# Optimization experiments

Hardware: AMD Instinct MI355X
Metric: run time of the kernel (lower is better)

## Reference

```python
import jax, jax.numpy as jnp
import numpy as np

N = 6144      # total residues (12 complexes x 512)
SEG = 512
NC = 14       # atom channels per residue
E = 64        # embed_size
HD = 128      # hidden_size
C = 25        # num_classes
K = 9         # k_neighbors
L = 3         # n_layers
ROUNDS = 3    # iter_round


def _forward(X, S, batch_id, embed, W_in, b_in, channel_w, eW1, eb1, eW2, eb2, cW1, cb1, cW2, cb2, nW1, nb1, nW2, nb2, mW1, mb1, mW2, mb2, oW1, ob1, oW2, ob2):
    n = X.shape[0]
    silu = jax.nn.silu
    # pairs in different complexes (or self) are never neighbors
    cross = (batch_id[:, None] != batch_id[None, :]) | jnp.eye(n, dtype=bool)
    Hmem = None
    H = None
    for t in range(ROUNDS):
        H0 = embed[S]                                    # residue embedding [N,E]
        if Hmem is not None:                             # keep_memory: memory_ffn(H_prev)
            m = silu(Hmem) @ mW1 + mb1
            H0 = H0 + (silu(m) @ mW2 + mb2)
        H = H0 @ W_in + b_in                             # [N,HD]
        # dynamic KNN edge construction on current CA coordinates (_knn_edges)
        ca = X[:, 1]                                     # [N,3]
        d2 = jnp.sum((ca[:, None, :] - ca[None, :, :]) ** 2, -1)
        d2 = jnp.where(cross, 1e9, d2)
        _, nbr = jax.lax.top_k(-d2, K)                   # [N,K] neighbor indices
        for l in range(L):                               # AMEGNN / AMEncoder layers
            Hj = H[nbr]                                  # gather [N,K,HD]
            Xj = X[nbr]                                  # gather [N,K,NC,3]
            diff = X[:, None] - Xj                       # [N,K,NC,3]
            # channel-weighted radial feature
            radial = jnp.einsum('nkcd,nkcd,c->nk', diff, diff, channel_w)[..., None]
            Hi = jnp.broadcast_to(H[:, None], Hj.shape)
            ein = jnp.concatenate([Hi, Hj, radial], -1)  # [N,K,2HD+1]
            msg = silu(silu(ein @ eW1[l] + eb1[l]) @ eW2[l] + eb2[l])
            scale = silu(msg @ cW1[l] + cb1[l]) @ cW2[l] + cb2[l]     # [N,K,1]
            X = X + jnp.mean(diff * scale[..., None], axis=1)        # equivariant coord update
            agg = jnp.sum(msg, axis=1)                   # scatter-sum over neighbors [N,HD]
            H = H + silu(jnp.concatenate([H, agg], -1) @ nW1[l] + nb1[l]) @ nW2[l] + nb2[l]
        Hmem = H
    logits = silu(silu(H) @ oW1 + ob1) @ oW2 + ob2       # ffn_residue
    return logits, X


def setup_inputs() -> dict:
    key = jax.random.key(0)
    ks = jax.random.split(key, 16)
    r = lambda i, shape, s=0.05: jax.random.normal(ks[i], shape, dtype=jnp.float32) * s
    return {
        'X': jax.random.normal(ks[0], (N, NC, 3), dtype=jnp.float32) * 3.0,
        'S': jax.random.randint(ks[1], (N,), 0, C),
        'batch_id': jnp.arange(N, dtype=jnp.int32) // SEG,
        'embed': r(2, (C, E), 1.0),
        'W_in': r(3, (E, HD)), 'b_in': jnp.zeros((HD,), jnp.float32),
        'channel_w': jax.random.uniform(ks[4], (NC,), dtype=jnp.float32),
        'eW1': r(5, (L, 2 * HD + 1, HD)), 'eb1': jnp.zeros((L, HD), jnp.float32),
        'eW2': r(6, (L, HD, HD)), 'eb2': jnp.zeros((L, HD), jnp.float32),
        'cW1': r(7, (L, HD, HD)), 'cb1': jnp.zeros((L, HD), jnp.float32),
        'cW2': r(8, (L, HD, 1)), 'cb2': jnp.zeros((L, 1), jnp.float32),
        'nW1': r(9, (L, 2 * HD, HD)), 'nb1': jnp.zeros((L, HD), jnp.float32),
        'nW2': r(10, (L, HD, HD)), 'nb2': jnp.zeros((L, HD), jnp.float32),
        'mW1': r(11, (HD, HD)), 'mb1': jnp.zeros((HD,), jnp.float32),
        'mW2': r(12, (HD, E)), 'mb2': jnp.zeros((E,), jnp.float32),
        'oW1': r(13, (HD, HD)), 'ob1': jnp.zeros((HD,), jnp.float32),
        'oW2': r(14, (HD, C)), 'ob2': jnp.zeros((C,), jnp.float32),
    }


def reference(X, S, batch_id, embed, W_in, b_in, channel_w, eW1, eb1, eW2, eb2, cW1, cb1, cW2, cb2, nW1, nb1, nW2, nb2, mW1, mb1, mW2, mb2, oW1, ob1, oW2, ob2):
    return _forward(X, S, batch_id, embed, W_in, b_in, channel_w, eW1, eb1, eW2, eb2, cW1, cb1, cW2, cb2, nW1, nb1, nW2, nb2, mW1, mb1, mW2, mb2, oW1, ob1, oW2, ob2)
```

## Files before the change

### kernel.cpp

```cpp
#include <hip/hip_runtime.h>
#include <math.h>

#define NNODE 6144
#define SEG   512
#define NCH   14
#define XD    42
#define ED    64
#define HD    128
#define NCLS  25
#define KN    9
#define NPB   7
#define ROWS  64
#define EDGE_BLOCKS ((NNODE + NPB - 1) / NPB)

typedef __attribute__((ext_vector_type(8))) short short8;
typedef __attribute__((ext_vector_type(4))) short short4v;
typedef __attribute__((ext_vector_type(4))) float f32x4;

__device__ __forceinline__ float silu_f(float x) {
  return x / (1.0f + __expf(-x));
}
__device__ __forceinline__ short f2bf(float x) {
  unsigned u = __builtin_bit_cast(unsigned, x);
  unsigned r = (u + 0x7fffu + ((u >> 16) & 1u)) >> 16;
  return (short)r;
}
__device__ __forceinline__ float bf2f(short s) {
  unsigned u = ((unsigned)(unsigned short)s) << 16;
  return __builtin_bit_cast(float, u);
}
__device__ __forceinline__ f32x4 mfma16(short8 a, short8 b, f32x4 c) {
  return __builtin_amdgcn_mfma_f32_16x16x32_bf16(a, b, c, 0, 0, 0);
}
__device__ __forceinline__ int swz128(int row, int col) {
  return row * 128 + (col ^ ((row & 7) << 3));
}
__device__ __forceinline__ int swz256(int row, int col) {
  return row * 256 + (col ^ ((row & 7) << 3));
}

__global__ __launch_bounds__(256) void prep_weights(
    const float* __restrict__ eW1, const float* __restrict__ eW2,
    const float* __restrict__ cW1, const float* __restrict__ nW1,
    const float* __restrict__ nW2, short* __restrict__ out)
{
  const int mat = blockIdx.y % 5, l = blockIdx.y / 5;
  const int idx = blockIdx.x * 256 + threadIdx.x;
  const int K = (mat == 0 || mat == 3) ? 256 : 128;
  if (idx >= K * 128) return;
  const int n = idx / K, k = idx - n * K;
  const float* src;
  switch (mat) {
    case 0: src = eW1 + (size_t)l * 257 * 128; break;
    case 1: src = eW2 + (size_t)l * 128 * 128; break;
    case 2: src = cW1 + (size_t)l * 128 * 128; break;
    case 3: src = nW1 + (size_t)l * 256 * 128; break;
    default: src = nW2 + (size_t)l * 128 * 128; break;
  }
  const int dofs[5] = {0, 32768, 49152, 65536, 98304};
  out[(size_t)l * 114688 + dofs[mat] + idx] = f2bf(src[k * 128 + n]);
}

__global__ void copy_kernel(const float* __restrict__ src, float* __restrict__ dst, int n) {
  int i = blockIdx.x * blockDim.x + threadIdx.x;
  if (i < n) dst[i] = src[i];
}

__global__ __launch_bounds__(512) void pq_kernel(
    const float* __restrict__ Hin, const short* __restrict__ W1T,
    float* __restrict__ PQ)
{
  __shared__ __align__(16) short A[16 * HD];
  const int t = threadIdx.x;
  const int m0 = blockIdx.x * 16;

  {
    const int r = t >> 5, c4 = t & 31;
    const float4 v = ((const float4*)(Hin + (size_t)m0 * HD))[r * 32 + c4];
    short4v s;
    s.x = f2bf(v.x); s.y = f2bf(v.y); s.z = f2bf(v.z); s.w = f2bf(v.w);
    *(short4v*)&A[swz128(r, c4 * 4)] = s;
  }
  __syncthreads();

  const int wid = t >> 6, lane = t & 63;
  const int lr = lane & 15, lk = lane >> 4;

  f32x4 acc[2] = {};
#pragma unroll
  for (int ks = 0; ks < 4; ++ks) {
    const int k0 = ks * 32 + lk * 8;
    const short8 a = *(const short8*)&A[swz128(lr, k0)];
#pragma unroll
    for (int ni = 0; ni < 2; ++ni) {
      const int c = (wid * 2 + ni) * 16 + lr;
      const short* bp = (c < HD) ? (W1T + c * 256 + k0)
                                 : (W1T + (c - HD) * 256 + HD + k0);
      const short8 b = *(const short8*)bp;
      acc[ni] = mfma16(a, b, acc[ni]);
    }
  }
#pragma unroll
  for (int ni = 0; ni < 2; ++ni) {
    const int c = (wid * 2 + ni) * 16 + lr;
#pragma unroll
    for (int g = 0; g < 4; ++g) {
      const int row = lk * 4 + g;
      PQ[(size_t)(m0 + row) * 256 + c] = acc[ni][g];
    }
  }
}

__global__ __launch_bounds__(128) void h_init_kernel(
    const float* __restrict__ embed, const int* __restrict__ S,
    const float* __restrict__ W_in, const float* __restrict__ b_in,
    const float* __restrict__ Hmem,
    const float* __restrict__ mW1, const float* __restrict__ mb1,
    const float* __restrict__ mW2, const float* __restrict__ mb2,
    float* __restrict__ Hout)
{
  __shared__ float a1[HD];
  __shared__ float a2[HD];
  __shared__ float h0[ED];
  const int i = blockIdx.x, j = threadIdx.x;

  if (Hmem) {
    a1[j] = silu_f(Hmem[i * HD + j]);
    __syncthreads();
    float m0 = 0.f, m1 = 0.f, m2 = 0.f, m3 = 0.f;
    for (int k = 0; k < HD; k += 4) {
      m0 = fmaf(a1[k + 0], mW1[(k + 0) * HD + j], m0);
      m1 = fmaf(a1[k + 1], mW1[(k + 1) * HD + j], m1);
      m2 = fmaf(a1[k + 2], mW1[(k + 2) * HD + j], m2);
      m3 = fmaf(a1[k + 3], mW1[(k + 3) * HD + j], m3);
    }
    a2[j] = silu_f(mb1[j] + ((m0 + m1) + (m2 + m3)));
    __syncthreads();
    if (j < ED) {
      float v0 = 0.f, v1 = 0.f, v2 = 0.f, v3 = 0.f;
      for (int k = 0; k < HD; k += 4) {
        v0 = fmaf(a2[k + 0], mW2[(k + 0) * ED + j], v0);
        v1 = fmaf(a2[k + 1], mW2[(k + 1) * ED + j], v1);
        v2 = fmaf(a2[k + 2], mW2[(k + 2) * ED + j], v2);
        v3 = fmaf(a2[k + 3], mW2[(k + 3) * ED + j], v3);
      }
      h0[j] = embed[S[i] * ED + j] + mb2[j] + ((v0 + v1) + (v2 + v3));
    }
  } else {
    if (j < ED) h0[j] = embed[S[i] * ED + j];
  }
  __syncthreads();
  float h0a = 0.f, h1a = 0.f, h2a = 0.f, h3a = 0.f;
  for (int k = 0; k < ED; k += 4) {
    h0a = fmaf(h0[k + 0], W_in[(k + 0) * HD + j], h0a);
    h1a = fmaf(h0[k + 1], W_in[(k + 1) * HD + j], h1a);
    h2a = fmaf(h0[k + 2], W_in[(k + 2) * HD + j], h2a);
    h3a = fmaf(h0[k + 3], W_in[(k + 3) * HD + j], h3a);
  }
  Hout[i * HD + j] = b_in[j] + ((h0a + h1a) + (h2a + h3a));
}

__global__ __launch_bounds__(256) void knn_kernel(const float* __restrict__ X,
                                                  int* __restrict__ nbr)
{
  const int w = threadIdx.x >> 6, lane = threadIdx.x & 63;
  const int i = blockIdx.x * 4 + w;
  const int base = (i / SEG) * SEG;

  const float cx = X[i * XD + 3], cy = X[i * XD + 4], cz = X[i * XD + 5];
  float dv[8];
  int   di[8];
#pragma unroll
  for (int q = 0; q < 8; ++q) {
    const int j = base + lane + q * 64;
    float dx = __fsub_rn(cx, X[j * XD + 3]);
    float dy = __fsub_rn(cy, X[j * XD + 4]);
    float dz = __fsub_rn(cz, X[j * XD + 5]);
    float d2 = __fadd_rn(__fadd_rn(__fmul_rn(dx, dx), __fmul_rn(dy, dy)), __fmul_rn(dz, dz));
    if (j == i) d2 = 1e9f;
    dv[q] = d2; di[q] = j;
  }
  for (int it = 0; it < KN; ++it) {
    float bv = dv[0]; int bi = di[0];
#pragma unroll
    for (int q = 1; q < 8; ++q)
      if (dv[q] < bv || (dv[q] == bv && di[q] < bi)) { bv = dv[q]; bi = di[q]; }
#pragma unroll
    for (int m = 1; m < 64; m <<= 1) {
      float ov = __shfl_xor(bv, m, 64);
      int   oi = __shfl_xor(bi, m, 64);
      if (ov < bv || (ov == bv && oi < bi)) { bv = ov; bi = oi; }
    }
    if (lane == 0) nbr[i * KN + it] = bi;
    const int rel = bi - base;
    const int oq = rel >> 6;
#pragma unroll
    for (int q = 0; q < 8; ++q)
      if (q == oq && (rel & 63) == lane) dv[q] = 3e38f;
  }
}

__global__ __launch_bounds__(512) void edge_layer_kernel(
    const float* __restrict__ Hin,  float* __restrict__ Hout,
    const float* __restrict__ Xin,  float* __restrict__ Xout,
    const int*   __restrict__ nbr,  const float* __restrict__ channel_w,
    const float* __restrict__ PQ,
    const float* __restrict__ eW1,  const float* __restrict__ eb1,
    const float* __restrict__ eb2,  const float* __restrict__ cb1,
    const float* __restrict__ cW2,  const float* __restrict__ cb2,
    const float* __restrict__ nb1,  const float* __restrict__ nb2,
    const short* __restrict__ W2T,  const short* __restrict__ C1T,
    const short* __restrict__ N1T,  const short* __restrict__ N2T)
{
  __shared__ __align__(16) short bufA[ROWS * HD];
  __shared__ __align__(16) short bufB[ROWS * HD];
  __shared__ __align__(16) short nodeA[NPB * 256];
  __shared__ __align__(16) short uT[NPB * HD];
  __shared__ float scalePart[ROWS][4];
  __shared__ int   nbrS[ROWS];

  const int t  = threadIdx.x;
  const int n0 = blockIdx.x * NPB;
  const int nvalid = (NNODE - n0 < NPB) ? (NNODE - n0) : NPB;
  const int evalid = nvalid * KN;

  {
    const int row  = t >> 3;
    const int part = t & 7;
    const bool rvalid = row < evalid;
    const int nd = row / KN;
    const int jn = rvalid ? nbr[n0 * KN + row] : n0;
    if (part == 0) nbrS[row] = jn;

    float r = 0.f;
    if (rvalid) {
      const float* xi = Xin + (size_t)(n0 + nd) * XD;
      const float* xj = Xin + (size_t)jn * XD;
      {
        const int c = part;
        float dx = xi[c * 3 + 0] - xj[c * 3 + 0];
        float dy = xi[c * 3 + 1] - xj[c * 3 + 1];
        float dz = xi[c * 3 + 2] - xj[c * 3 + 2];
        r += channel_w[c] * (dx * dx + dy * dy + dz * dz);
      }
      if (part < 6) {
        const int c = part + 8;
        float dx = xi[c * 3 + 0] - xj[c * 3 + 0];
        float dy = xi[c * 3 + 1] - xj[c * 3 + 1];
        float dz = xi[c * 3 + 2] - xj[c * 3 + 2];
        r += channel_w[c] * (dx * dx + dy * dy + dz * dz);
      }
    }
    r += __shfl_xor(r, 1, 64);
    r += __shfl_xor(r, 2, 64);
    r += __shfl_xor(r, 4, 64);

    if (t < NPB * (HD / 4)) {
      const int r2 = t >> 5, c4 = t & 31;
      float4 v = make_float4(0.f, 0.f, 0.f, 0.f);
      if (r2 < nvalid) v = ((const float4*)Hin)[(size_t)(n0 + r2) * 32 + c4];
      short4v s;
      s.x = f2bf(v.x); s.y = f2bf(v.y); s.z = f2bf(v.z); s.w = f2bf(v.w);
      *(short4v*)&nodeA[swz256(r2, c4 * 4)] = s;
    }

    const int inode = n0 + ((nd < nvalid) ? nd : 0);
    const float4* PQ4 = (const float4*)PQ;
    const float4* w2564 = (const float4*)(eW1 + 256 * HD);
    const float4* eb14 = (const float4*)eb1;
#pragma unroll
    for (int ii = 0; ii < 4; ++ii) {
      const int c4 = part + ii * 8;
      const float4 p = PQ4[(size_t)inode * 64 + c4];
      const float4 q = PQ4[(size_t)jn * 64 + 32 + c4];
      const float4 w = w2564[c4];
      const float4 bb = eb14[c4];
      short4v s;
      s.x = f2bf(silu_f(p.x + q.x + r * w.x + bb.x));
      s.y = f2bf(silu_f(p.y + q.y + r * w.y + bb.y));
      s.z = f2bf(silu_f(p.z + q.z + r * w.z + bb.z));
      s.w = f2bf(silu_f(p.w + q.w + r * w.w + bb.w));
      *(short4v*)&bufA[swz128(row, c4 * 4)] = s;
    }
  }
  __syncthreads();

  const int wid  = t >> 6;
  const int lane = t & 63;
  const int m2 = wid >> 2;
  const int n2 = wid & 3;
  const int lr = lane & 15;
  const int lk = lane >> 4;
  const int rA0 = (m2 * 2) * 16 + lr;
  const int rA1 = rA0 + 16;

  {
    f32x4 acc[2][2] = {};
    const short* b0p = W2T + ((n2 * 2) * 16 + lr) * 128;
    const short* b1p = b0p + 16 * 128;
#pragma unroll
    for (int ks = 0; ks < 4; ++ks) {
      const int k0 = ks * 32 + lk * 8;
      const short8 a0 = *(const short8*)&bufA[swz128(rA0, k0)];
      const short8 a1 = *(const short8*)&bufA[swz128(rA1, k0)];
      const short8 b0 = *(const short8*)(b0p + k0);
      const short8 b1 = *(const short8*)(b1p + k0);
      acc[0][0] = mfma16(a0, b0, acc[0][0]);
      acc[0][1] = mfma16(a0, b1, acc[0][1]);
      acc[1][0] = mfma16(a1, b0, acc[1][0]);
      acc[1][1] = mfma16(a1, b1, acc[1][1]);
    }
#pragma unroll
    for (int ni = 0; ni < 2; ++ni) {
      const int col = (n2 * 2 + ni) * 16 + lr;
      const float bias = eb2[col];
#pragma unroll
      for (int mi = 0; mi < 2; ++mi) {
        const int rb = (m2 * 2 + mi) * 16 + lk * 4;
#pragma unroll
        for (int g = 0; g < 4; ++g)
          bufB[swz128(rb + g, col)] = f2bf(silu_f(acc[mi][ni][g] + bias));
      }
    }
  }
  __syncthreads();

  {
    f32x4 acc[2][2] = {};
    const short* b0p = C1T + ((n2 * 2) * 16 + lr) * 128;
    const short* b1p = b0p + 16 * 128;
#pragma unroll
    for (int ks = 0; ks < 4; ++ks) {
      const int k0 = ks * 32 + lk * 8;
      const short8 a0 = *(const short8*)&bufB[swz128(rA0, k0)];
      const short8 a1 = *(const short8*)&bufB[swz128(rA1, k0)];
      const short8 b0 = *(const short8*)(b0p + k0);
      const short8 b1 = *(const short8*)(b1p + k0);
      acc[0][0] = mfma16(a0, b0, acc[0][0]);
      acc[0][1] = mfma16(a0, b1, acc[0][1]);
      acc[1][0] = mfma16(a1, b0, acc[1][0]);
      acc[1][1] = mfma16(a1, b1, acc[1][1]);
    }
    float p[2][4];
#pragma unroll
    for (int mi = 0; mi < 2; ++mi)
#pragma unroll
      for (int g = 0; g < 4; ++g) p[mi][g] = 0.f;
#pragma unroll
    for (int ni = 0; ni < 2; ++ni) {
      const int col = (n2 * 2 + ni) * 16 + lr;
      const float bias = cb1[col];
      const float wv = cW2[col];
#pragma unroll
      for (int mi = 0; mi < 2; ++mi)
#pragma unroll
        for (int g = 0; g < 4; ++g)
          p[mi][g] = fmaf(silu_f(acc[mi][ni][g] + bias), wv, p[mi][g]);
    }
#pragma unroll
    for (int m = 1; m < 16; m <<= 1) {
#pragma unroll
      for (int mi = 0; mi < 2; ++mi)
#pragma unroll
        for (int g = 0; g < 4; ++g)
          p[mi][g] += __shfl_xor(p[mi][g], m, 64);
    }
    if (lr == 0) {
#pragma unroll
      for (int mi = 0; mi < 2; ++mi)
#pragma unroll
        for (int g = 0; g < 4; ++g)
          scalePart[(m2 * 2 + mi) * 16 + lk * 4 + g][n2] = p[mi][g];
    }
  }
  for (int idx = t; idx < NPB * HD; idx += 512) {
    const int r2 = idx >> 7, col = idx & 127;
    float v = 0.f;
    if (r2 < nvalid) {
#pragma unroll
      for (int k = 0; k < KN; ++k) v += bf2f(bufB[swz128(r2 * KN + k, col)]);
    }
    nodeA[swz256(r2, col + HD)] = f2bf(v);
  }
  __syncthreads();

  {
    f32x4 acc = {};
    const short* bp = N1T + (wid * 16 + lr) * 256;
#pragma unroll
    for (int ks = 0; ks < 8; ++ks) {
      const int k0 = ks * 32 + lk * 8;
      short8 a = {0, 0, 0, 0, 0, 0, 0, 0};
      if (lr < NPB) a = *(const short8*)&nodeA[swz256(lr, k0)];
      const short8 b = *(const short8*)(bp + k0);
      acc = mfma16(a, b, acc);
    }
    const int col = wid * 16 + lr;
    const float bias = nb1[col];
#pragma unroll
    for (int g = 0; g < 4; ++g) {
      const int orow = lk * 4 + g;
      if (orow < NPB) uT[swz128(orow, col)] = f2bf(silu_f(acc[g] + bias));
    }
  }
  {
    const float c2 = cb2[0];
    for (int idx = t; idx < NPB * XD; idx += 512) {
      const int nd = idx / XD, e = idx - nd * XD;
      if (nd < nvalid) {
        const float xi = Xin[(size_t)n0 * XD + idx];
        float a = 0.f;
#pragma unroll
        for (int k = 0; k < KN; ++k) {
          const int r = nd * KN + k;
          const float sc = ((scalePart[r][0] + scalePart[r][1])
                          + (scalePart[r][2] + scalePart[r][3])) + c2;
          a += (xi - Xin[(size_t)nbrS[r] * XD + e]) * sc;
        }
        Xout[(size_t)(n0 + nd) * XD + e] = xi + a / 9.0f;
      }
    }
  }
  __syncthreads();

  {
    f32x4 acc = {};
    const short* bp = N2T + (wid * 16 + lr) * 128;
#pragma unroll
    for (int ks = 0; ks < 4; ++ks) {
      const int k0 = ks * 32 + lk * 8;
      short8 a = {0, 0, 0, 0, 0, 0, 0, 0};
      if (lr < NPB) a = *(const short8*)&uT[swz128(lr, k0)];
      const short8 b = *(const short8*)(bp + k0);
      acc = mfma16(a, b, acc);
    }
    const int col = wid * 16 + lr;
    const float bias = nb2[col];
#pragma unroll
    for (int g = 0; g < 4; ++g) {
      const int row = lk * 4 + g;
      if (row < nvalid)
        Hout[(size_t)(n0 + row) * HD + col] =
            Hin[(size_t)(n0 + row) * HD + col] + acc[g] + bias;
    }
  }
}

__global__ __launch_bounds__(128) void out_kernel(
    const float* __restrict__ H, const float* __restrict__ X,
    const float* __restrict__ oW1, const float* __restrict__ ob1,
    const float* __restrict__ oW2, const float* __restrict__ ob2,
    float* __restrict__ out)
{
  __shared__ float hs[HD];
  __shared__ float u[HD];
  const int i = blockIdx.x, j = threadIdx.x;

  hs[j] = silu_f(H[i * HD + j]);
  __syncthreads();
  float a0 = 0.f, a1 = 0.f, a2 = 0.f, a3 = 0.f;
  for (int k = 0; k < HD; k += 4) {
    a0 = fmaf(hs[k + 0], oW1[(k + 0) * HD + j], a0);
    a1 = fmaf(hs[k + 1], oW1[(k + 1) * HD + j], a1);
    a2 = fmaf(hs[k + 2], oW1[(k + 2) * HD + j], a2);
    a3 = fmaf(hs[k + 3], oW1[(k + 3) * HD + j], a3);
  }
  u[j] = silu_f(ob1[j] + ((a0 + a1) + (a2 + a3)));
  __syncthreads();
  if (j < NCLS) {
    float o0 = 0.f, o1 = 0.f, o2 = 0.f, o3 = 0.f;
    for (int k = 0; k < HD; k += 4) {
      o0 = fmaf(u[k + 0], oW2[(k + 0) * NCLS + j], o0);
      o1 = fmaf(u[k + 1], oW2[(k + 1) * NCLS + j], o1);
      o2 = fmaf(u[k + 2], oW2[(k + 2) * NCLS + j], o2);
      o3 = fmaf(u[k + 3], oW2[(k + 3) * NCLS + j], o3);
    }
    out[i * NCLS + j] = ob2[j] + ((o0 + o1) + (o2 + o3));
  }
  if (j < XD) out[NNODE * NCLS + i * XD + j] = X[i * XD + j];
}

extern "C" void kernel_launch(void* const* d_in, const int* in_sizes, int n_in,
                              void* d_out, int out_size, void* d_ws, size_t ws_size,
                              hipStream_t stream)
{
  const float* X0       = (const float*)d_in[0];
  const int*   S        = (const int*)  d_in[1];
  const float* embed    = (const float*)d_in[3];
  const float* W_in     = (const float*)d_in[4];
  const float* b_in     = (const float*)d_in[5];
  const float* channelw = (const float*)d_in[6];
  const float* eW1      = (const float*)d_in[7];
  const float* eb1      = (const float*)d_in[8];
  const float* eW2      = (const float*)d_in[9];
  const float* eb2      = (const float*)d_in[10];
  const float* cW1      = (const float*)d_in[11];
  const float* cb1      = (const float*)d_in[12];
  const float* cW2      = (const float*)d_in[13];
  const float* cb2      = (const float*)d_in[14];
  const float* nW1      = (const float*)d_in[15];
  const float* nb1      = (const float*)d_in[16];
  const float* nW2      = (const float*)d_in[17];
  const float* nb2      = (const float*)d_in[18];
  const float* mW1      = (const float*)d_in[19];
  const float* mb1      = (const float*)d_in[20];
  const float* mW2      = (const float*)d_in[21];
  const float* mb2      = (const float*)d_in[22];
  const float* oW1      = (const float*)d_in[23];
  const float* ob1      = (const float*)d_in[24];
  const float* oW2      = (const float*)d_in[25];
  const float* ob2      = (const float*)d_in[26];

  char* ws = (char*)d_ws;
  const size_t HBYTES = (size_t)NNODE * HD * sizeof(float);
  const size_t XBYTES = (size_t)NNODE * XD * sizeof(float);
  float* Hb[2] = { (float*)(ws), (float*)(ws + HBYTES) };
  float* Xb[2] = { (float*)(ws + 2 * HBYTES), (float*)(ws + 2 * HBYTES + XBYTES) };
  int*   nbr   = (int*)(ws + 2 * HBYTES + 2 * XBYTES);
  short* Wbf   = (short*)(ws + 2 * HBYTES + 2 * XBYTES + (size_t)NNODE * KN * sizeof(int));
  float* PQ    = (float*)(ws + 2 * HBYTES + 2 * XBYTES + (size_t)NNODE * KN * sizeof(int)
                             + 3 * 114688 * sizeof(short));

  prep_weights<<<dim3(128, 15), 256, 0, stream>>>(eW1, eW2, cW1, nW1, nW2, Wbf);
  copy_kernel<<<(NNODE * XD + 255) / 256, 256, 0, stream>>>(X0, Xb[0], NNODE * XD);

  int hc = 0, xc = 0;
  for (int t = 0; t < 3; ++t) {
    const float* Hmem = (t == 0) ? nullptr : Hb[hc];
    h_init_kernel<<<NNODE, HD, 0, stream>>>(embed, S, W_in, b_in, Hmem,
                                            mW1, mb1, mW2, mb2, Hb[hc ^ 1]);
    hc ^= 1;
    knn_kernel<<<NNODE / 4, 256, 0, stream>>>(Xb[xc], nbr);
    for (int l = 0; l < 3; ++l) {
      const short* Wl = Wbf + (size_t)l * 114688;
      pq_kernel<<<NNODE / 16, 512, 0, stream>>>(Hb[hc], Wl, PQ);
      edge_layer_kernel<<<EDGE_BLOCKS, 512, 0, stream>>>(
          Hb[hc], Hb[hc ^ 1], Xb[xc], Xb[xc ^ 1], nbr, channelw, PQ,
          eW1 + (size_t)l * 257 * HD, eb1 + (size_t)l * HD,
          eb2 + (size_t)l * HD,  cb1 + (size_t)l * HD,
          cW2 + (size_t)l * HD,  cb2 + (size_t)l,
          nb1 + (size_t)l * HD,  nb2 + (size_t)l * HD,
          Wl + 32768, Wl + 49152, Wl + 65536, Wl + 98304);
      hc ^= 1; xc ^= 1;
    }
  }
  out_kernel<<<NNODE, HD, 0, stream>>>(Hb[hc], Xb[xc], oW1, ob1, oW2, ob2, (float*)d_out);
}
```

Before: 595.5 us.

## Fuse PQ projection into h_init and edge layers, MFMA h_init, bf16 PQ

Replaces the per-residue scalar h_init kernel with a 16-row MFMA kernel that also computes the first layer's PQ projection. Each edge layer now computes the next layer's PQ from its output H while still in shared memory, which removes the separate pq_kernel launches. PQ is stored in bf16 to halve gather traffic, and knn uses 8 waves per block. The costs are extra work in the edge kernel tail, reuse of shared buffer space, and added bf16 rounding of PQ and the memory MLP.

Result: faster. 535.3 us (-10.1%).

```diff
diff --git a/kernel.cpp b/kernel.cpp
--- a/kernel.cpp
+++ b/kernel.cpp
@@ -38,14 +38,37 @@
 __device__ __forceinline__ int swz256(int row, int col) {
   return row * 256 + (col ^ ((row & 7) << 3));
 }
+__device__ __forceinline__ int swz64(int row, int col) {
+  return row * 64 + (col ^ ((row & 7) << 3));
+}
+
+#define EXOFF 344064
+#define WBF_SHORTS (EXOFF + 32768)
 
 __global__ __launch_bounds__(256) void prep_weights(
     const float* __restrict__ eW1, const float* __restrict__ eW2,
     const float* __restrict__ cW1, const float* __restrict__ nW1,
-    const float* __restrict__ nW2, short* __restrict__ out)
+    const float* __restrict__ nW2, const float* __restrict__ mW1,
+    const float* __restrict__ mW2, const float* __restrict__ W_in,
+    short* __restrict__ out)
 {
+  const int idx = blockIdx.x * 256 + threadIdx.x;
+  if (blockIdx.y == 15) {
+    if (idx < 16384) {
+      const int n = idx >> 7, k = idx & 127;
+      out[EXOFF + idx] = f2bf(mW1[k * HD + n]);
+    } else if (idx < 24576) {
+      const int local = idx - 16384;
+      const int n = local >> 7, k = local & 127;
+      out[EXOFF + 16384 + local] = f2bf(mW2[k * ED + n]);
+    } else if (idx < 32768) {
+      const int local = idx - 24576;
+      const int n = local >> 6, k = local & 63;
+      out[EXOFF + 24576 + local] = f2bf(W_in[k * HD + n]);
+    }
+    return;
+  }
   const int mat = blockIdx.y % 5, l = blockIdx.y / 5;
-  const int idx = blockIdx.x * 256 + threadIdx.x;
   const int K = (mat == 0 || mat == 3) ? 256 : 128;
   if (idx >= K * 128) return;
   const int n = idx / K, k = idx - n * K;
@@ -66,105 +89,128 @@
   if (i < n) dst[i] = src[i];
 }
 
-__global__ __launch_bounds__(512) void pq_kernel(
-    const float* __restrict__ Hin, const short* __restrict__ W1T,
-    float* __restrict__ PQ)
+__global__ __launch_bounds__(512) void h_init_mfma(
+    const float* __restrict__ embed, const int* __restrict__ S,
+    const short* __restrict__ W_inT, const float* __restrict__ b_in,
+    const float* __restrict__ Hmem,
+    const short* __restrict__ mW1T, const float* __restrict__ mb1,
+    const short* __restrict__ mW2T, const float* __restrict__ mb2,
+    const short* __restrict__ W1T0,
+    float* __restrict__ Hout, short* __restrict__ PQ0)
 {
   __shared__ __align__(16) short A[16 * HD];
+  __shared__ __align__(16) short Bu[16 * HD];
+  __shared__ __align__(16) short h0B[16 * ED];
+  __shared__ __align__(16) short HB[16 * HD];
   const int t = threadIdx.x;
   const int m0 = blockIdx.x * 16;
-
-  {
-    const int r = t >> 5, c4 = t & 31;
-    const float4 v = ((const float4*)(Hin + (size_t)m0 * HD))[r * 32 + c4];
-    short4v s;
-    s.x = f2bf(v.x); s.y = f2bf(v.y); s.z = f2bf(v.z); s.w = f2bf(v.w);
-    *(short4v*)&A[swz128(r, c4 * 4)] = s;
-  }
-  __syncthreads();
-
-  const int wid = t >> 6, lane = t & 63;
-  const int lr = lane & 15, lk = lane >> 4;
-
-  f32x4 acc[2] = {};
-#pragma unroll
-  for (int ks = 0; ks < 4; ++ks) {
-    const int k0 = ks * 32 + lk * 8;
-    const short8 a = *(const short8*)&A[swz128(lr, k0)];
+  const int wid = t >> 6, lane = t & 63, lr = lane & 15, lk = lane >> 4;
+
+  if (Hmem) {
+    {
+      const int r = t >> 5, c4 = t & 31;
+      const float4 v = ((const float4*)Hmem)[(size_t)(m0 + r) * 32 + c4];
+      short4v s;
+      s.x = f2bf(silu_f(v.x)); s.y = f2bf(silu_f(v.y));
+      s.z = f2bf(silu_f(v.z)); s.w = f2bf(silu_f(v.w));
+      *(short4v*)&A[swz128(r, c4 * 4)] = s;
+    }
+    __syncthreads();
+    {
+      f32x4 acc[2] = {};
+#pragma unroll
+      for (int ks = 0; ks < 4; ++ks) {
+        const int k0 = ks * 32 + lk * 8;
+        const short8 a = *(const short8*)&A[swz128(lr, k0)];
+#pragma unroll
+        for (int ni = 0; ni < 2; ++ni) {
+          const int c = (wid * 2 + ni) * 16 + lr;
+          acc[ni] = mfma16(a, *(const short8*)(mW1T + c * 128 + k0), acc[ni]);
+        }
+      }
+#pragma unroll
+      for (int ni = 0; ni < 2; ++ni) {
+        const int col = (wid * 2 + ni) * 16 + lr;
+        const float bias = mb1[col];
+#pragma unroll
+        for (int g = 0; g < 4; ++g)
+          Bu[swz128(lk * 4 + g, col)] = f2bf(silu_f(acc[ni][g] + bias));
+      }
+    }
+    __syncthreads();
+    if (wid < 4) {
+      f32x4 acc = {};
+#pragma unroll
+      for (int ks = 0; ks < 4; ++ks) {
+        const int k0 = ks * 32 + lk * 8;
+        const short8 a = *(const short8*)&Bu[swz128(lr, k0)];
+        const int c = wid * 16 + lr;
+        acc = mfma16(a, *(const short8*)(mW2T + c * 128 + k0), acc);
+      }
+      const int col = wid * 16 + lr;
+      const float bias = mb2[col];
+#pragma unroll
+      for (int g = 0; g < 4; ++g) {
+        const int row = lk * 4 + g;
+        h0B[swz64(row, col)] = f2bf(embed[S[m0 + row] * ED + col] + acc[g] + bias);
+      }
+    }
+  } else {
+    for (int idx = t; idx < 16 * ED; idx += 512) {
+      const int row = idx >> 6, col = idx & 63;
+      h0B[swz64(row, col)] = f2bf(embed[S[m0 + row] * ED + col]);
+    }
+  }
+  __syncthreads();
+  {
+    f32x4 acc = {};
+#pragma unroll
+    for (int ks = 0; ks < 2; ++ks) {
+      const int k0 = ks * 32 + lk * 8;
+      const short8 a = *(const short8*)&h0B[swz64(lr, k0)];
+      const int c = wid * 16 + lr;
+      acc = mfma16(a, *(const short8*)(W_inT + c * 64 + k0), acc);
+    }
+    const int col = wid * 16 + lr;
+    const float bias = b_in[col];
+#pragma unroll
+    for (int g = 0; g < 4; ++g) {
+      const int row = lk * 4 + g;
+      const float hv = acc[g] + bias;
+      Hout[(size_t)(m0 + row) * HD + col] = hv;
+      HB[swz128(row, col)] = f2bf(hv);
+    }
+  }
+  __syncthreads();
+  {
+    f32x4 acc[2] = {};
+#pragma unroll
+    for (int ks = 0; ks < 4; ++ks) {
+      const int k0 = ks * 32 + lk * 8;
+      const short8 a = *(const short8*)&HB[swz128(lr, k0)];
+#pragma unroll
+      for (int ni = 0; ni < 2; ++ni) {
+        const int c = (wid * 2 + ni) * 16 + lr;
+        const short* bp = (c < HD) ? (W1T0 + c * 256 + k0)
+                                   : (W1T0 + (c - HD) * 256 + HD + k0);
+        acc[ni] = mfma16(a, *(const short8*)bp, acc[ni]);
+      }
+    }
 #pragma unroll
     for (int ni = 0; ni < 2; ++ni) {
       const int c = (wid * 2 + ni) * 16 + lr;
-      const short* bp = (c < HD) ? (W1T + c * 256 + k0)
-                                 : (W1T + (c - HD) * 256 + HD + k0);
-      const short8 b = *(const short8*)bp;
-      acc[ni] = mfma16(a, b, acc[ni]);
-    }
-  }
-#pragma unroll
-  for (int ni = 0; ni < 2; ++ni) {
-    const int c = (wid * 2 + ni) * 16 + lr;
-#pragma unroll
-    for (int g = 0; g < 4; ++g) {
-      const int row = lk * 4 + g;
-      PQ[(size_t)(m0 + row) * 256 + c] = acc[ni][g];
-    }
-  }
-}
-
-__global__ __launch_bounds__(128) void h_init_kernel(
-    const float* __restrict__ embed, const int* __restrict__ S,
-    const float* __restrict__ W_in, const float* __restrict__ b_in,
-    const float* __restrict__ Hmem,
-    const float* __restrict__ mW1, const float* __restrict__ mb1,
-    const float* __restrict__ mW2, const float* __restrict__ mb2,
-    float* __restrict__ Hout)
-{
-  __shared__ float a1[HD];
-  __shared__ float a2[HD];
-  __shared__ float h0[ED];
-  const int i = blockIdx.x, j = threadIdx.x;
-
-  if (Hmem) {
-    a1[j] = silu_f(Hmem[i * HD + j]);
-    __syncthreads();
-    float m0 = 0.f, m1 = 0.f, m2 = 0.f, m3 = 0.f;
-    for (int k = 0; k < HD; k += 4) {
-      m0 = fmaf(a1[k + 0], mW1[(k + 0) * HD + j], m0);
-      m1 = fmaf(a1[k + 1], mW1[(k + 1) * HD + j], m1);
-      m2 = fmaf(a1[k + 2], mW1[(k + 2) * HD + j], m2);
-      m3 = fmaf(a1[k + 3], mW1[(k + 3) * HD + j], m3);
-    }
-    a2[j] = silu_f(mb1[j] + ((m0 + m1) + (m2 + m3)));
-    __syncthreads();
-    if (j < ED) {
-      float v0 = 0.f, v1 = 0.f, v2 = 0.f, v3 = 0.f;
-      for (int k = 0; k < HD; k += 4) {
-        v0 = fmaf(a2[k + 0], mW2[(k + 0) * ED + j], v0);
-        v1 = fmaf(a2[k + 1], mW2[(k + 1) * ED + j], v1);
-        v2 = fmaf(a2[k + 2], mW2[(k + 2) * ED + j], v2);
-        v3 = fmaf(a2[k + 3], mW2[(k + 3) * ED + j], v3);
-      }
-      h0[j] = embed[S[i] * ED + j] + mb2[j] + ((v0 + v1) + (v2 + v3));
-    }
-  } else {
-    if (j < ED) h0[j] = embed[S[i] * ED + j];
-  }
-  __syncthreads();
-  float h0a = 0.f, h1a = 0.f, h2a = 0.f, h3a = 0.f;
-  for (int k = 0; k < ED; k += 4) {
-    h0a = fmaf(h0[k + 0], W_in[(k + 0) * HD + j], h0a);
-    h1a = fmaf(h0[k + 1], W_in[(k + 1) * HD + j], h1a);
-    h2a = fmaf(h0[k + 2], W_in[(k + 2) * HD + j], h2a);
-    h3a = fmaf(h0[k + 3], W_in[(k + 3) * HD + j], h3a);
-  }
-  Hout[i * HD + j] = b_in[j] + ((h0a + h1a) + (h2a + h3a));
-}
-
-__global__ __launch_bounds__(256) void knn_kernel(const float* __restrict__ X,
+#pragma unroll
+      for (int g = 0; g < 4; ++g)
+        PQ0[(size_t)(m0 + lk * 4 + g) * 256 + c] = f2bf(acc[ni][g]);
+    }
+  }
+}
+
+__global__ __launch_bounds__(512) void knn_kernel(const float* __restrict__ X,
                                                   int* __restrict__ nbr)
 {
   const int w = threadIdx.x >> 6, lane = threadIdx.x & 63;
-  const int i = blockIdx.x * 4 + w;
+  const int i = blockIdx.x * 8 + w;
   const int base = (i / SEG) * SEG;
 
   const float cx = X[i * XD + 3], cy = X[i * XD + 4], cz = X[i * XD + 5];
@@ -204,13 +250,14 @@
     const float* __restrict__ Hin,  float* __restrict__ Hout,
     const float* __restrict__ Xin,  float* __restrict__ Xout,
     const int*   __restrict__ nbr,  const float* __restrict__ channel_w,
-    const float* __restrict__ PQ,
+    const short* __restrict__ PQ,
     const float* __restrict__ eW1,  const float* __restrict__ eb1,
     const float* __restrict__ eb2,  const float* __restrict__ cb1,
     const float* __restrict__ cW2,  const float* __restrict__ cb2,
     const float* __restrict__ nb1,  const float* __restrict__ nb2,
     const short* __restrict__ W2T,  const short* __restrict__ C1T,
-    const short* __restrict__ N1T,  const short* __restrict__ N2T)
+    const short* __restrict__ N1T,  const short* __restrict__ N2T,
+    const short* __restrict__ W1Tn, short* __restrict__ PQn)
 {
   __shared__ __align__(16) short bufA[ROWS * HD];
   __shared__ __align__(16) short bufB[ROWS * HD];
@@ -218,6 +265,7 @@
   __shared__ __align__(16) short uT[NPB * HD];
   __shared__ float scalePart[ROWS][4];
   __shared__ int   nbrS[ROWS];
+  short* houtB = bufA;
 
   const int t  = threadIdx.x;
   const int n0 = blockIdx.x * NPB;
@@ -265,21 +313,21 @@
     }
 
     const int inode = n0 + ((nd < nvalid) ? nd : 0);
-    const float4* PQ4 = (const float4*)PQ;
+    const short4v* PQv = (const short4v*)PQ;
     const float4* w2564 = (const float4*)(eW1 + 256 * HD);
     const float4* eb14 = (const float4*)eb1;
 #pragma unroll
     for (int ii = 0; ii < 4; ++ii) {
       const int c4 = part + ii * 8;
-      const float4 p = PQ4[(size_t)inode * 64 + c4];
-      const float4 q = PQ4[(size_t)jn * 64 + 32 + c4];
+      const short4v ps = PQv[(size_t)inode * 64 + c4];
+      const short4v qs = PQv[(size_t)jn * 64 + 32 + c4];
       const float4 w = w2564[c4];
       const float4 bb = eb14[c4];
       short4v s;
-      s.x = f2bf(silu_f(p.x + q.x + r * w.x + bb.x));
-      s.y = f2bf(silu_f(p.y + q.y + r * w.y + bb.y));
-      s.z = f2bf(silu_f(p.z + q.z + r * w.z + bb.z));
-      s.w = f2bf(silu_f(p.w + q.w + r * w.w + bb.w));
+      s.x = f2bf(silu_f(bf2f(ps.x) + bf2f(qs.x) + r * w.x + bb.x));
+      s.y = f2bf(silu_f(bf2f(ps.y) + bf2f(qs.y) + r * w.y + bb.y));
+      s.z = f2bf(silu_f(bf2f(ps.z) + bf2f(qs.z) + r * w.z + bb.z));
+      s.w = f2bf(silu_f(bf2f(ps.w) + bf2f(qs.w) + r * w.w + bb.w));
       *(short4v*)&bufA[swz128(row, c4 * 4)] = s;
     }
   }
@@ -439,9 +487,38 @@
 #pragma unroll
     for (int g = 0; g < 4; ++g) {
       const int row = lk * 4 + g;
-      if (row < nvalid)
-        Hout[(size_t)(n0 + row) * HD + col] =
-            Hin[(size_t)(n0 + row) * HD + col] + acc[g] + bias;
+      if (row < nvalid) {
+        const float hv = Hin[(size_t)(n0 + row) * HD + col] + acc[g] + bias;
+        Hout[(size_t)(n0 + row) * HD + col] = hv;
+        if (W1Tn) houtB[swz128(row, col)] = f2bf(hv);
+      }
+    }
+  }
+
+  if (W1Tn) {
+    __syncthreads();
+    f32x4 acc[2] = {};
+#pragma unroll
+    for (int ks = 0; ks < 4; ++ks) {
+      const int k0 = ks * 32 + lk * 8;
+      short8 a = {0, 0, 0, 0, 0, 0, 0, 0};
+      if (lr < NPB) a = *(const short8*)&houtB[swz128(lr, k0)];
+#pragma unroll
+      for (int ni = 0; ni < 2; ++ni) {
+        const int c = (wid * 2 + ni) * 16 + lr;
+        const short* bp = (c < HD) ? (W1Tn + c * 256 + k0)
+                                   : (W1Tn + (c - HD) * 256 + HD + k0);
+        acc[ni] = mfma16(a, *(const short8*)bp, acc[ni]);
+      }
+    }
+#pragma unroll
+    for (int ni = 0; ni < 2; ++ni) {
+      const int c = (wid * 2 + ni) * 16 + lr;
+#pragma unroll
+      for (int g = 0; g < 4; ++g) {
+        const int row = lk * 4 + g;
+        if (row < nvalid) PQn[(size_t)(n0 + row) * 256 + c] = f2bf(acc[ni][g]);
+      }
     }
   }
 }
@@ -514,33 +591,42 @@
   char* ws = (char*)d_ws;
   const size_t HBYTES = (size_t)NNODE * HD * sizeof(float);
   const size_t XBYTES = (size_t)NNODE * XD * sizeof(float);
+  const size_t NBRB   = (size_t)NNODE * KN * sizeof(int);
+  const size_t WBFB   = (size_t)WBF_SHORTS * sizeof(short);
+  const size_t PQB    = (size_t)NNODE * 256 * sizeof(short);
   float* Hb[2] = { (float*)(ws), (float*)(ws + HBYTES) };
   float* Xb[2] = { (float*)(ws + 2 * HBYTES), (float*)(ws + 2 * HBYTES + XBYTES) };
   int*   nbr   = (int*)(ws + 2 * HBYTES + 2 * XBYTES);
-  short* Wbf   = (short*)(ws + 2 * HBYTES + 2 * XBYTES + (size_t)NNODE * KN * sizeof(int));
-  float* PQ    = (float*)(ws + 2 * HBYTES + 2 * XBYTES + (size_t)NNODE * KN * sizeof(int)
-                             + 3 * 114688 * sizeof(short));
-
-  prep_weights<<<dim3(128, 15), 256, 0, stream>>>(eW1, eW2, cW1, nW1, nW2, Wbf);
+  short* Wbf   = (short*)(ws + 2 * HBYTES + 2 * XBYTES + NBRB);
+  short* PQb[2] = { (short*)(ws + 2 * HBYTES + 2 * XBYTES + NBRB + WBFB),
+                    (short*)(ws + 2 * HBYTES + 2 * XBYTES + NBRB + WBFB + PQB) };
+
+  prep_weights<<<dim3(128, 16), 256, 0, stream>>>(eW1, eW2, cW1, nW1, nW2,
+                                                  mW1, mW2, W_in, Wbf);
   copy_kernel<<<(NNODE * XD + 255) / 256, 256, 0, stream>>>(X0, Xb[0], NNODE * XD);
 
   int hc = 0, xc = 0;
   for (int t = 0; t < 3; ++t) {
     const float* Hmem = (t == 0) ? nullptr : Hb[hc];
-    h_init_kernel<<<NNODE, HD, 0, stream>>>(embed, S, W_in, b_in, Hmem,
-                                            mW1, mb1, mW2, mb2, Hb[hc ^ 1]);
+    h_init_mfma<<<NNODE / 16, 512, 0, stream>>>(
+        embed, S, Wbf + EXOFF + 24576, b_in, Hmem,
+        Wbf + EXOFF, mb1, Wbf + EXOFF + 16384, mb2,
+        Wbf , Hb[hc ^ 1], PQb[0]);
     hc ^= 1;
-    knn_kernel<<<NNODE / 4, 256, 0, stream>>>(Xb[xc], nbr);
+    knn_kernel<<<NNODE / 8, 512, 0, stream>>>(Xb[xc], nbr);
     for (int l = 0; l < 3; ++l) {
       const short* Wl = Wbf + (size_t)l * 114688;
-      pq_kernel<<<NNODE / 16, 512, 0, stream>>>(Hb[hc], Wl, PQ);
+      const short* Wn = (l < 2) ? (Wbf + (size_t)(l + 1) * 114688) : nullptr;
+      const short* pqr = (l == 1) ? PQb[1] : PQb[0];
+      short* pqw = (l == 0) ? PQb[1] : ((l == 1) ? PQb[0] : nullptr);
       edge_layer_kernel<<<EDGE_BLOCKS, 512, 0, stream>>>(
-          Hb[hc], Hb[hc ^ 1], Xb[xc], Xb[xc ^ 1], nbr, channelw, PQ,
+          Hb[hc], Hb[hc ^ 1], Xb[xc], Xb[xc ^ 1], nbr, channelw, pqr,
           eW1 + (size_t)l * 257 * HD, eb1 + (size_t)l * HD,
           eb2 + (size_t)l * HD,  cb1 + (size_t)l * HD,
           cW2 + (size_t)l * HD,  cb2 + (size_t)l,
           nb1 + (size_t)l * HD,  nb2 + (size_t)l * HD,
-          Wl + 32768, Wl + 49152, Wl + 65536, Wl + 98304);
+          Wl + 32768, Wl + 49152, Wl + 65536, Wl + 98304,
+          Wn, pqw);
       hc ^= 1; xc ^= 1;
     }
   }
```
